# Kernel optimization log

Hardware: AMD Instinct MI355X
Metric: run time of the kernel (lower is better)

## Reference

```python
import jax, jax.numpy as jnp
import numpy as np

SEQ, BATCH, IN, H = 188, 256, 128, 256


def _lstm_scan(x_proj, w_hh, batch, hidden):
    # x_proj: (T, B, 4H) = input projection + biases, already computed
    h0 = jnp.zeros((batch, hidden), x_proj.dtype)
    c0 = jnp.zeros((batch, hidden), x_proj.dtype)
    w_hh_t = w_hh.T  # (H, 4H)

    def step(carry, xt):
        h, c = carry
        gates = xt + h @ w_hh_t  # (B, 4H)
        i, f, g, o = jnp.split(gates, 4, axis=-1)  # PyTorch gate order i,f,g,o
        i = jax.nn.sigmoid(i)
        f = jax.nn.sigmoid(f)
        g = jnp.tanh(g)
        o = jax.nn.sigmoid(o)
        c = f * c + i * g
        h = o * jnp.tanh(c)
        return (h, c), h

    _, hs = jax.lax.scan(step, (h0, c0), x_proj)
    return hs  # (T, B, H)


def setup_inputs() -> dict:
    key = jax.random.key(0)
    ks = jax.random.split(key, 9)
    s = 1.0 / np.sqrt(H)  # PyTorch default init scale
    mk = lambda k, shape: jax.random.uniform(k, shape, jnp.float32, -s, s)
    return {
        "x": jax.random.normal(ks[0], (SEQ, BATCH, IN), jnp.float32),
        "w_ih_f": mk(ks[1], (4 * H, IN)),
        "w_hh_f": mk(ks[2], (4 * H, H)),
        "b_ih_f": mk(ks[3], (4 * H,)),
        "b_hh_f": mk(ks[4], (4 * H,)),
        "w_ih_b": mk(ks[5], (4 * H, IN)),
        "w_hh_b": mk(ks[6], (4 * H, H)),
        "b_ih_b": mk(ks[7], (4 * H,)),
        "b_hh_b": mk(ks[8], (4 * H,)),
    }


def reference(x, w_ih_f, w_hh_f, b_ih_f, b_hh_f, w_ih_b, w_hh_b, b_ih_b, b_hh_b):
    batch = x.shape[1]
    # Precompute input projections for all timesteps (big GEMM outside the scan)
    xp_f = jnp.einsum('tbi,gi->tbg', x, w_ih_f) + b_ih_f + b_hh_f
    xp_b = jnp.einsum('tbi,gi->tbg', x[::-1], w_ih_b) + b_ih_b + b_hh_b
    out_f = _lstm_scan(xp_f, w_hh_f, batch, H)            # (T, B, H)
    out_b = _lstm_scan(xp_b, w_hh_b, batch, H)[::-1]      # reversed back
    return jnp.concatenate([out_f, out_b], axis=-1)       # (T, B, 2H)
```

## Files before the change

kernel.cpp:

```cpp
#include <hip/hip_runtime.h>

#define T_SEQ 188
#define NB    256
#define NIN   128
#define NH    256
#define SCQ   (0.0625f / 16129.0f)

typedef __attribute__((ext_vector_type(8))) short s16x8;
typedef __attribute__((ext_vector_type(4))) short s16x4;
typedef __attribute__((ext_vector_type(4))) float f32x4;
typedef __attribute__((ext_vector_type(4))) int   i32x4;

__device__ __forceinline__ short f2bf(float f) {
    union { float f; unsigned u; } v; v.f = f;
    unsigned r = v.u + 0x7fffu + ((v.u >> 16) & 1u);
    return (short)(r >> 16);
}
__device__ __forceinline__ float bf2f(unsigned short s) {
    union { unsigned u; float f; } t; t.u = ((unsigned)s) << 16; return t.f;
}
__device__ __forceinline__ float sigf(float x) {
    return __builtin_amdgcn_rcpf(1.0f + __expf(-x));
}
__device__ __forceinline__ float tanh_(float x) {
    return 1.0f - 2.0f * __builtin_amdgcn_rcpf(__expf(2.0f * x) + 1.0f);
}

__device__ __forceinline__ void lds_barrier() {
    asm volatile("s_waitcnt lgkmcnt(0)" ::: "memory");
    __builtin_amdgcn_s_barrier();
    asm volatile("" ::: "memory");
}

__global__ __launch_bounds__(256) void xp_gemm(
    const float* __restrict__ x,
    const float* __restrict__ w_ih_f, const float* __restrict__ w_ih_b,
    const float* __restrict__ b_ih_f, const float* __restrict__ b_hh_f,
    const float* __restrict__ b_ih_b, const float* __restrict__ b_hh_b,
    unsigned short* __restrict__ xp)
{
    const int mt = blockIdx.x >> 1;
    const int d  = blockIdx.x & 1;
    const int t  = mt >> 2, b0 = (mt & 3) * 64;
    const float* w_ih = d ? w_ih_b : w_ih_f;
    const float* b_ih = d ? b_ih_b : b_ih_f;
    const float* b_hh = d ? b_hh_b : b_hh_f;
    const int tid = threadIdx.x;
    const int v = tid >> 6, l = tid & 63, lg = l >> 4, lb = l & 15;

    __shared__ short wl[64][136];
    __shared__ float biasS[1024];

    #pragma unroll
    for (int j = 0; j < 4; ++j) {
        const int g = tid * 4 + j * 1024; (void)g;
    }
    {
        const int g = tid * 4;
        float4 bi = *(const float4*)(b_ih + g);
        float4 bh = *(const float4*)(b_hh + g);
        biasS[g + 0] = bi.x + bh.x; biasS[g + 1] = bi.y + bh.y;
        biasS[g + 2] = bi.z + bh.z; biasS[g + 3] = bi.w + bh.w;
    }

    s16x8 a[4];
    {
        const float* xr = x + ((size_t)(t * NB + b0 + 16 * v + lb)) * NIN + 8 * lg;
        #pragma unroll
        for (int kk = 0; kk < 4; ++kk) {
            float4 p0 = *(const float4*)(xr + 32 * kk);
            float4 p1 = *(const float4*)(xr + 32 * kk + 4);
            s16x8 tv;
            tv[0] = f2bf(p0.x); tv[1] = f2bf(p0.y); tv[2] = f2bf(p0.z); tv[3] = f2bf(p0.w);
            tv[4] = f2bf(p1.x); tv[5] = f2bf(p1.y); tv[6] = f2bf(p1.z); tv[7] = f2bf(p1.w);
            a[kk] = tv;
        }
    }

    const int wr = tid >> 2, wk = (tid & 3) * 32;

    unsigned short* xpb =
        xp + ((size_t)(d * T_SEQ + t) * NB + b0 + 16 * v + 4 * lg) * 1024 + lb;

    for (int nt = 0; nt < 16; ++nt) {
        const int Nb = nt * 64;
        {
            const float* wsrc = w_ih + ((size_t)(Nb + wr)) * NIN + wk;
            #pragma unroll
            for (int j = 0; j < 4; ++j) {
                float4 p0 = *(const float4*)(wsrc + 8 * j);
                float4 p1 = *(const float4*)(wsrc + 8 * j + 4);
                s16x8 tv;
                tv[0] = f2bf(p0.x); tv[1] = f2bf(p0.y); tv[2] = f2bf(p0.z); tv[3] = f2bf(p0.w);
                tv[4] = f2bf(p1.x); tv[5] = f2bf(p1.y); tv[6] = f2bf(p1.z); tv[7] = f2bf(p1.w);
                *(s16x8*)&wl[wr][wk + 8 * j] = tv;
            }
        }
        __syncthreads();

        f32x4 acc[4];
        #pragma unroll
        for (int nf = 0; nf < 4; ++nf) {
            const float bs = biasS[Nb + nf * 16 + lb];
            acc[nf][0] = bs; acc[nf][1] = bs; acc[nf][2] = bs; acc[nf][3] = bs;
        }
        #pragma unroll
        for (int kk = 0; kk < 4; ++kk)
            #pragma unroll
            for (int nf = 0; nf < 4; ++nf) {
                s16x8 bf_ = *(const s16x8*)&wl[nf * 16 + lb][kk * 32 + 8 * lg];
                acc[nf] = __builtin_amdgcn_mfma_f32_16x16x32_bf16(a[kk], bf_, acc[nf], 0, 0, 0);
            }
        __syncthreads();

        #pragma unroll
        for (int nf = 0; nf < 4; ++nf)
            #pragma unroll
            for (int rr = 0; rr < 4; ++rr)
                xpb[(size_t)rr * 1024 + Nb + nf * 16] = (unsigned short)f2bf(acc[nf][rr]);
    }
}

__device__ __forceinline__ void lstm_step(
    int p, int w, int l, int lg, int lb, int c, int huq, int hwb,
    const unsigned short*& xpp, long dxp, float*& outp, long dout,
    int* hl, int (&rscr)[16][4][4][16],
    const i32x4 (&wq)[4][4], float& cst,
    unsigned short (&cur)[4], unsigned short (&nxt)[4])
{
    #pragma unroll
    for (int G = 0; G < 4; ++G)
        nxt[G] = xpp[G * 256];
    xpp += dxp;

    i32x4 ac[4];
    #pragma unroll
    for (int G = 0; G < 4; ++G) {
        ac[G][0] = 0; ac[G][1] = 0; ac[G][2] = 0; ac[G][3] = 0;
    }
    #pragma unroll
    for (int kk = 0; kk < 4; ++kk) {
        i32x4 bq = *(const i32x4*)&hl[p * 1024 + kk * 256 + 4 * l];
        ac[0] = __builtin_amdgcn_mfma_i32_16x16x64_i8(wq[0][kk], bq, ac[0], 0, 0, 0);
        ac[1] = __builtin_amdgcn_mfma_i32_16x16x64_i8(wq[1][kk], bq, ac[1], 0, 0, 0);
        ac[2] = __builtin_amdgcn_mfma_i32_16x16x64_i8(wq[2][kk], bq, ac[2], 0, 0, 0);
        ac[3] = __builtin_amdgcn_mfma_i32_16x16x64_i8(wq[3][kk], bq, ac[3], 0, 0, 0);
    }

    if (lb < 4) {
        #pragma unroll
        for (int G = 0; G < 4; ++G)
            *(i32x4*)&rscr[w][G][lb][4 * lg] = ac[G];
    }
    asm volatile("s_waitcnt lgkmcnt(0)" ::: "memory");
    int av[4];
    #pragma unroll
    for (int G = 0; G < 4; ++G)
        av[G] = rscr[w][G][c][huq];
    asm volatile("s_waitcnt lgkmcnt(0)" ::: "memory");

    const float gi = SCQ * (float)av[0] + bf2f(cur[0]);
    const float gf = SCQ * (float)av[1] + bf2f(cur[1]);
    const float gg = SCQ * (float)av[2] + bf2f(cur[2]);
    const float go = SCQ * (float)av[3] + bf2f(cur[3]);
    const float iv = sigf(gi), fv = sigf(gf);
    const float gv = tanh_(gg), ov = sigf(go);
    const float cc = fv * cst + iv * gv;
    cst = cc;
    const float h = ov * tanh_(cc);
    *outp = h;
    outp += dout;
    ((signed char*)hl)[(p ^ 1) * 4096 + hwb] = (signed char)(int)rintf(h * 127.0f);

    lds_barrier();
}

__global__ __launch_bounds__(1024, 4) void lstm_rec(
    const float* __restrict__ w_hh_f, const float* __restrict__ w_hh_b,
    const unsigned short* __restrict__ xp, float* __restrict__ out)
{
    const int bid = blockIdx.x;
    const int d  = bid >> 6;
    const int bt = bid & 63;
    const float* w_hh = d ? w_hh_b : w_hh_f;
    const int tid = threadIdx.x;
    const int w = tid >> 6, l = tid & 63, lg = l >> 4, lb = l & 15;
    const int c = l & 3, huq = l >> 2;

    __shared__ int hl[2 * 1024];
    __shared__ int rscr[16][4][4][16];

    i32x4 wq[4][4];
    #pragma unroll
    for (int G = 0; G < 4; ++G) {
        const int row = G * 256 + 16 * w + lb;
        #pragma unroll
        for (int kk = 0; kk < 4; ++kk) {
            i32x4 pk;
            #pragma unroll
            for (int r = 0; r < 4; ++r) {
                float4 wv = *(const float4*)(w_hh + (size_t)row * NH + kk * 64 + 16 * lg + 4 * r);
                const int q0 = (int)rintf(wv.x * 2032.0f) & 255;
                const int q1 = (int)rintf(wv.y * 2032.0f) & 255;
                const int q2 = (int)rintf(wv.z * 2032.0f) & 255;
                const int q3 = (int)rintf(wv.w * 2032.0f) & 255;
                pk[r] = q0 | (q1 << 8) | (q2 << 16) | (q3 << 24);
            }
            wq[G][kk] = pk;
        }
    }
    for (int i = tid; i < 2048; i += 1024) hl[i] = 0;

    const int hu = 16 * w + huq;
    const int hwb = (hu >> 6) * 1024 + ((hu >> 4) & 3) * 256 + c * 16 + (hu & 15);

    float cst = 0.f;
    unsigned short XPA[4], XPB[4];
    const int t0 = d ? (T_SEQ - 1) : 0;
    const long dxp  = (d ? -(long)NB : (long)NB) * 1024;
    const long dout = (d ? -(long)NB : (long)NB) * 512;
    const unsigned short* xpp =
        xp + ((size_t)(d * T_SEQ + t0) * NB + bt * 4 + c) * 1024 + hu;
    float* outp = out + ((size_t)t0 * NB + bt * 4 + c) * 512 + d * 256 + hu;
    #pragma unroll
    for (int G = 0; G < 4; ++G)
        XPA[G] = xpp[G * 256];
    xpp += dxp;
    __syncthreads();

    for (int s2 = 0; s2 < T_SEQ / 2; ++s2) {
        lstm_step(0, w, l, lg, lb, c, huq, hwb, xpp, dxp, outp, dout,
                  hl, rscr, wq, cst, XPA, XPB);
        lstm_step(1, w, l, lg, lb, c, huq, hwb, xpp, dxp, outp, dout,
                  hl, rscr, wq, cst, XPB, XPA);
    }
}

#define ZSTR_FB 392
__global__ __launch_bounds__(512, 2) void lstm_fb(
    const float* __restrict__ x,
    const float* __restrict__ w_ih_f, const float* __restrict__ w_hh_f,
    const float* __restrict__ b_ih_f, const float* __restrict__ b_hh_f,
    const float* __restrict__ w_ih_b, const float* __restrict__ w_hh_b,
    const float* __restrict__ b_ih_b, const float* __restrict__ b_hh_b,
    float* __restrict__ out, unsigned* __restrict__ flags)
{
    const int b  = blockIdx.x;
    const int d  = b >> 5;
    const int hh = (b >> 4) & 1;
    const int bt = b & 15;
    const int pb = b ^ 16;
    const int po = 1 - hh;
    const float* w_ih = d ? w_ih_b : w_ih_f;
    const float* w_hh = d ? w_hh_b : w_hh_f;
    const float* b_ih = d ? b_ih_b : b_ih_f;
    const float* b_hh = d ? b_hh_b : b_hh_f;
    const int tid = threadIdx.x;
    const int w = tid >> 6, l = tid & 63, lg = l >> 4, lb = l & 15;
    const int hbase = hh * 128 + 16 * w;

    __shared__ short Z[2][16][ZSTR_FB];
    __shared__ float biasL[8][4][16];
    const int off_x   = lg * 8;
    const int off_own = (4 + 4 * hh) * 32 + lg * 8;
    const int off_par = (4 + 4 * po) * 32 + lg * 8;

    s16x8 wf[4][12];
    #pragma unroll
    for (int G = 0; G < 4; ++G) {
        const int gc = G * 256 + hbase + lb;
        #pragma unroll
        for (int kkidx = 0; kkidx < 12; ++kkidx) {
            const int kb = (kkidx < 4) ? (off_x + 32 * kkidx)
                         : (kkidx < 8) ? (off_own + 32 * (kkidx - 4))
                                       : (off_par + 32 * (kkidx - 8));
            const float* src = (kb < NIN) ? (w_ih + (size_t)gc * NIN + kb)
                                          : (w_hh + (size_t)gc * NH + (kb - NIN));
            float4 a  = *(const float4*)(src);
            float4 b2 = *(const float4*)(src + 4);
            s16x8 tv;
            tv[0] = f2bf(a.x);  tv[1] = f2bf(a.y);  tv[2] = f2bf(a.z);  tv[3] = f2bf(a.w);
            tv[4] = f2bf(b2.x); tv[5] = f2bf(b2.y); tv[6] = f2bf(b2.z); tv[7] = f2bf(b2.w);
            wf[G][kkidx] = tv;
        }
    }
    {
        const int G = lb >> 2, r = lb & 3;
        const int gcr = G * 256 + hbase + 4 * lg + r;
        biasL[w][G][4 * lg + r] = b_ih[gcr] + b_hh[gcr];
    }
    const int srow = tid >> 5;
    const int sk4  = (tid & 31) * 4;
    {
        s16x8 zz;
        #pragma unroll
        for (int i = 0; i < 8; ++i) zz[i] = 0;
        *(s16x8*)&Z[0][srow][NIN + (tid & 31) * 8] = zz;
        const int t0 = d ? (T_SEQ - 1) : 0;
        float4 xv0 = *(const float4*)(x + ((size_t)(t0 * NB + bt * 16 + srow)) * NIN + sk4);
        s16x4 xp_;
        xp_[0] = f2bf(xv0.x); xp_[1] = f2bf(xv0.y); xp_[2] = f2bf(xv0.z); xp_[3] = f2bf(xv0.w);
        *(s16x4*)&Z[0][srow][sk4] = xp_;
    }
    float cst[4] = {0.f, 0.f, 0.f, 0.f};
    __syncthreads();
    unsigned* myflag = flags + b * 16;
    unsigned* pflag  = flags + pb * 16;
    float* outp = out + (size_t)(bt * 16) * 512 + d * 256 + hbase + 4 * lg;

    for (int s = 0; s < T_SEQ; ++s) {
        const int p = s & 1;
        const int t = d ? (T_SEQ - 1 - s) : s;
        float4 xv;
        const bool havex = (s + 1 < T_SEQ);
        if (havex) {
            const int tn = d ? (T_SEQ - 2 - s) : (s + 1);
            xv = *(const float4*)(x + ((size_t)(tn * NB + bt * 16 + srow)) * NIN + sk4);
        }
        f32x4 acc[4];
        #pragma unroll
        for (int G = 0; G < 4; ++G)
            acc[G] = *(const f32x4*)&biasL[w][G][4 * lg];
        const short* zrow = &Z[p][lb][0];
        #pragma unroll
        for (int kk = 0; kk < 4; ++kk) {
            s16x8 bfv = *(const s16x8*)(zrow + off_x + 32 * kk);
            acc[0] = __builtin_amdgcn_mfma_f32_16x16x32_bf16(wf[0][kk], bfv, acc[0], 0, 0, 0);
            acc[1] = __builtin_amdgcn_mfma_f32_16x16x32_bf16(wf[1][kk], bfv, acc[1], 0, 0, 0);
            acc[2] = __builtin_amdgcn_mfma_f32_16x16x32_bf16(wf[2][kk], bfv, acc[2], 0, 0, 0);
            acc[3] = __builtin_amdgcn_mfma_f32_16x16x32_bf16(wf[3][kk], bfv, acc[3], 0, 0, 0);
        }
        #pragma unroll
        for (int kk = 0; kk < 4; ++kk) {
            s16x8 bfv = *(const s16x8*)(zrow + off_own + 32 * kk);
            acc[0] = __builtin_amdgcn_mfma_f32_16x16x32_bf16(wf[0][4 + kk], bfv, acc[0], 0, 0, 0);
            acc[1] = __builtin_amdgcn_mfma_f32_16x16x32_bf16(wf[1][4 + kk], bfv, acc[1], 0, 0, 0);
            acc[2] = __builtin_amdgcn_mfma_f32_16x16x32_bf16(wf[2][4 + kk], bfv, acc[2], 0, 0, 0);
            acc[3] = __builtin_amdgcn_mfma_f32_16x16x32_bf16(wf[3][4 + kk], bfv, acc[3], 0, 0, 0);
        }
        if (s > 0) {
            const unsigned want = (unsigned)s;
            while (__hip_atomic_load(pflag, __ATOMIC_RELAXED, __HIP_MEMORY_SCOPE_AGENT) < want)
                __builtin_amdgcn_s_sleep(1);
            __builtin_amdgcn_fence(__ATOMIC_ACQUIRE, "agent");
            const int tprev = d ? (T_SEQ - s) : (s - 1);
            float4 pv = *(const float4*)(out + (size_t)tprev * NB * 512
                         + (size_t)(bt * 16 + srow) * 512 + d * 256 + po * 128 + sk4);
            s16x4 pp;
            pp[0] = f2bf(pv.x); pp[1] = f2bf(pv.y); pp[2] = f2bf(pv.z); pp[3] = f2bf(pv.w);
            *(s16x4*)&Z[p][srow][NIN + po * 128 + sk4] = pp;
        }
        __syncthreads();
        #pragma unroll
        for (int kk = 0; kk < 4; ++kk) {
            s16x8 bfv = *(const s16x8*)(zrow + off_par + 32 * kk);
            acc[0] = __builtin_amdgcn_mfma_f32_16x16x32_bf16(wf[0][8 + kk], bfv, acc[0], 0, 0, 0);
            acc[1] = __builtin_amdgcn_mfma_f32_16x16x32_bf16(wf[1][8 + kk], bfv, acc[1], 0, 0, 0);
            acc[2] = __builtin_amdgcn_mfma_f32_16x16x32_bf16(wf[2][8 + kk], bfv, acc[2], 0, 0, 0);
            acc[3] = __builtin_amdgcn_mfma_f32_16x16x32_bf16(wf[3][8 + kk], bfv, acc[3], 0, 0, 0);
        }
        float4 hout; s16x4 hbf;
        #pragma unroll
        for (int r = 0; r < 4; ++r) {
            const float iv = sigf(acc[0][r]);
            const float fv = sigf(acc[1][r]);
            const float gv = tanh_(acc[2][r]);
            const float ov = sigf(acc[3][r]);
            const float cc = fv * cst[r] + iv * gv;
            cst[r] = cc;
            const float h = ov * tanh_(cc);
            (&hout.x)[r] = h;
            hbf[r] = f2bf(h);
        }
        *(s16x4*)&Z[p ^ 1][lb][NIN + hbase + 4 * lg] = hbf;
        if (havex) {
            s16x4 xp_;
            xp_[0] = f2bf(xv.x); xp_[1] = f2bf(xv.y); xp_[2] = f2bf(xv.z); xp_[3] = f2bf(xv.w);
            *(s16x4*)&Z[p ^ 1][srow][sk4] = xp_;
        }
        *(f32x4*)(outp + (size_t)t * NB * 512 + lb * 512) = *(f32x4*)&hout;
        __syncthreads();
        if (tid == 0 && s + 1 < T_SEQ)
            __hip_atomic_store(myflag, (unsigned)(s + 1),
                               __ATOMIC_RELEASE, __HIP_MEMORY_SCOPE_AGENT);
    }
}

extern "C" void kernel_launch(void* const* d_in, const int* in_sizes, int n_in,
                              void* d_out, int out_size, void* d_ws, size_t ws_size,
                              hipStream_t stream) {
    const float* x      = (const float*)d_in[0];
    const float* w_ih_f = (const float*)d_in[1];
    const float* w_hh_f = (const float*)d_in[2];
    const float* b_ih_f = (const float*)d_in[3];
    const float* b_hh_f = (const float*)d_in[4];
    const float* w_ih_b = (const float*)d_in[5];
    const float* w_hh_b = (const float*)d_in[6];
    const float* b_ih_b = (const float*)d_in[7];
    const float* b_hh_b = (const float*)d_in[8];
    float* out = (float*)d_out;

    const size_t XPN = (size_t)2 * T_SEQ * NB * 1024;

    if (ws_size >= XPN * 2) {
        unsigned short* xp = (unsigned short*)d_ws;
        xp_gemm<<<dim3(752 * 2), dim3(256), 0, stream>>>(
            x, w_ih_f, w_ih_b, b_ih_f, b_hh_f, b_ih_b, b_hh_b, xp);
        lstm_rec<<<dim3(128), dim3(1024), 0, stream>>>(w_hh_f, w_hh_b, xp, out);
    } else {
        unsigned* flags = (unsigned*)d_ws;
        hipMemsetAsync(flags, 0, 4096, stream);
        lstm_fb<<<dim3(64), dim3(512), 0, stream>>>(
            x, w_ih_f, w_hh_f, b_ih_f, b_hh_f, w_ih_b, w_hh_b, b_ih_b, b_hh_b,
            out, flags);
    }
}
```

Measured before the change: 346.3 us.

## Fuse input-projection GEMM into recurrent kernel with flag-based producer/consumer overlap

Merges the separate xp_gemm and lstm_rec launches into one kernel. The first 128 blocks run the recurrence, and the remaining blocks compute input projections in time order for each direction. Producers publish per-timestep, per-batch-group flags, and recurrent blocks spin-wait on them in chunks of 32 steps, so the GEMM overlaps the serial recurrence instead of running before it. It also stages the GEMM output through LDS so global stores are coalesced. The cost is a memset plus polling overhead, and the scheme relies on the 128 recurrent blocks being co-resident with the producers to avoid deadlock. GEMM blocks now launch 1024 threads while only 256 do work, so they waste occupancy.

Measured after the change: 522.3 us. 1.51x slower.

```diff
diff --git a/kernel.cpp b/kernel.cpp
--- a/kernel.cpp
+++ b/kernel.cpp
@@ -5,6 +5,7 @@
 #define NIN   128
 #define NH    256
 #define SCQ   (0.0625f / 16129.0f)
+#define NREC  128
 
 typedef __attribute__((ext_vector_type(8))) short s16x8;
 typedef __attribute__((ext_vector_type(4))) short s16x4;
@@ -25,106 +26,16 @@
 __device__ __forceinline__ float tanh_(float x) {
     return 1.0f - 2.0f * __builtin_amdgcn_rcpf(__expf(2.0f * x) + 1.0f);
 }
-
 __device__ __forceinline__ void lds_barrier() {
     asm volatile("s_waitcnt lgkmcnt(0)" ::: "memory");
     __builtin_amdgcn_s_barrier();
     asm volatile("" ::: "memory");
 }
 
-__global__ __launch_bounds__(256) void xp_gemm(
-    const float* __restrict__ x,
-    const float* __restrict__ w_ih_f, const float* __restrict__ w_ih_b,
-    const float* __restrict__ b_ih_f, const float* __restrict__ b_hh_f,
-    const float* __restrict__ b_ih_b, const float* __restrict__ b_hh_b,
-    unsigned short* __restrict__ xp)
-{
-    const int mt = blockIdx.x >> 1;
-    const int d  = blockIdx.x & 1;
-    const int t  = mt >> 2, b0 = (mt & 3) * 64;
-    const float* w_ih = d ? w_ih_b : w_ih_f;
-    const float* b_ih = d ? b_ih_b : b_ih_f;
-    const float* b_hh = d ? b_hh_b : b_hh_f;
-    const int tid = threadIdx.x;
-    const int v = tid >> 6, l = tid & 63, lg = l >> 4, lb = l & 15;
-
-    __shared__ short wl[64][136];
-    __shared__ float biasS[1024];
-
-    #pragma unroll
-    for (int j = 0; j < 4; ++j) {
-        const int g = tid * 4 + j * 1024; (void)g;
-    }
-    {
-        const int g = tid * 4;
-        float4 bi = *(const float4*)(b_ih + g);
-        float4 bh = *(const float4*)(b_hh + g);
-        biasS[g + 0] = bi.x + bh.x; biasS[g + 1] = bi.y + bh.y;
-        biasS[g + 2] = bi.z + bh.z; biasS[g + 3] = bi.w + bh.w;
-    }
-
-    s16x8 a[4];
-    {
-        const float* xr = x + ((size_t)(t * NB + b0 + 16 * v + lb)) * NIN + 8 * lg;
-        #pragma unroll
-        for (int kk = 0; kk < 4; ++kk) {
-            float4 p0 = *(const float4*)(xr + 32 * kk);
-            float4 p1 = *(const float4*)(xr + 32 * kk + 4);
-            s16x8 tv;
-            tv[0] = f2bf(p0.x); tv[1] = f2bf(p0.y); tv[2] = f2bf(p0.z); tv[3] = f2bf(p0.w);
-            tv[4] = f2bf(p1.x); tv[5] = f2bf(p1.y); tv[6] = f2bf(p1.z); tv[7] = f2bf(p1.w);
-            a[kk] = tv;
-        }
-    }
-
-    const int wr = tid >> 2, wk = (tid & 3) * 32;
-
-    unsigned short* xpb =
-        xp + ((size_t)(d * T_SEQ + t) * NB + b0 + 16 * v + 4 * lg) * 1024 + lb;
-
-    for (int nt = 0; nt < 16; ++nt) {
-        const int Nb = nt * 64;
-        {
-            const float* wsrc = w_ih + ((size_t)(Nb + wr)) * NIN + wk;
-            #pragma unroll
-            for (int j = 0; j < 4; ++j) {
-                float4 p0 = *(const float4*)(wsrc + 8 * j);
-                float4 p1 = *(const float4*)(wsrc + 8 * j + 4);
-                s16x8 tv;
-                tv[0] = f2bf(p0.x); tv[1] = f2bf(p0.y); tv[2] = f2bf(p0.z); tv[3] = f2bf(p0.w);
-                tv[4] = f2bf(p1.x); tv[5] = f2bf(p1.y); tv[6] = f2bf(p1.z); tv[7] = f2bf(p1.w);
-                *(s16x8*)&wl[wr][wk + 8 * j] = tv;
-            }
-        }
-        __syncthreads();
-
-        f32x4 acc[4];
-        #pragma unroll
-        for (int nf = 0; nf < 4; ++nf) {
-            const float bs = biasS[Nb + nf * 16 + lb];
-            acc[nf][0] = bs; acc[nf][1] = bs; acc[nf][2] = bs; acc[nf][3] = bs;
-        }
-        #pragma unroll
-        for (int kk = 0; kk < 4; ++kk)
-            #pragma unroll
-            for (int nf = 0; nf < 4; ++nf) {
-                s16x8 bf_ = *(const s16x8*)&wl[nf * 16 + lb][kk * 32 + 8 * lg];
-                acc[nf] = __builtin_amdgcn_mfma_f32_16x16x32_bf16(a[kk], bf_, acc[nf], 0, 0, 0);
-            }
-        __syncthreads();
-
-        #pragma unroll
-        for (int nf = 0; nf < 4; ++nf)
-            #pragma unroll
-            for (int rr = 0; rr < 4; ++rr)
-                xpb[(size_t)rr * 1024 + Nb + nf * 16] = (unsigned short)f2bf(acc[nf][rr]);
-    }
-}
-
 __device__ __forceinline__ void lstm_step(
     int p, int w, int l, int lg, int lb, int c, int huq, int hwb,
     const unsigned short*& xpp, long dxp, float*& outp, long dout,
-    int* hl, int (&rscr)[16][4][4][16],
+    int* hl, int (*rscr)[4][4][16],
     const i32x4 (&wq)[4][4], float& cst,
     unsigned short (&cur)[4], unsigned short (&nxt)[4])
 {
@@ -175,20 +86,127 @@
     lds_barrier();
 }
 
-__global__ __launch_bounds__(1024, 4) void lstm_rec(
-    const float* __restrict__ w_hh_f, const float* __restrict__ w_hh_b,
-    const unsigned short* __restrict__ xp, float* __restrict__ out)
+__global__ __launch_bounds__(1024, 4) void lstm_fused(
+    const float* __restrict__ x,
+    const float* __restrict__ w_ih_f, const float* __restrict__ w_hh_f,
+    const float* __restrict__ b_ih_f, const float* __restrict__ b_hh_f,
+    const float* __restrict__ w_ih_b, const float* __restrict__ w_hh_b,
+    const float* __restrict__ b_ih_b, const float* __restrict__ b_hh_b,
+    unsigned short* __restrict__ xp, int* __restrict__ flags,
+    float* __restrict__ out)
 {
+    __shared__ char smem[30208];
     const int bid = blockIdx.x;
+    const int tid = threadIdx.x;
+
+    if (bid >= NREC) {
+        const int gid = bid - NREC;
+        const int d   = gid & 1;
+        const int mt  = gid >> 1;
+        const int tseq = mt >> 2, g = mt & 3;
+        const int t   = d ? (T_SEQ - 1 - tseq) : tseq;
+        const int b0  = g * 64;
+        const float* w_ih = d ? w_ih_b : w_ih_f;
+        const float* b_ih = d ? b_ih_b : b_ih_f;
+        const float* b_hh = d ? b_hh_b : b_hh_f;
+
+        if (tid >= 256) {
+            for (int i = 0; i < 33; ++i) __syncthreads();
+            return;
+        }
+
+        short (*wl)[136]  = (short(*)[136])smem;
+        short (*xo)[68]   = (short(*)[68])(smem + 17408);
+        float* biasS      = (float*)(smem + 26112);
+
+        const int v = tid >> 6, l = tid & 63, lg = l >> 4, lb = l & 15;
+        {
+            const int gg4 = tid * 4;
+            float4 bi = *(const float4*)(b_ih + gg4);
+            float4 bh = *(const float4*)(b_hh + gg4);
+            biasS[gg4 + 0] = bi.x + bh.x; biasS[gg4 + 1] = bi.y + bh.y;
+            biasS[gg4 + 2] = bi.z + bh.z; biasS[gg4 + 3] = bi.w + bh.w;
+        }
+        s16x8 a[4];
+        {
+            const float* xr = x + ((size_t)(t * NB + b0 + 16 * v + lb)) * NIN + 8 * lg;
+            #pragma unroll
+            for (int kk = 0; kk < 4; ++kk) {
+                float4 p0 = *(const float4*)(xr + 32 * kk);
+                float4 p1 = *(const float4*)(xr + 32 * kk + 4);
+                s16x8 tv;
+                tv[0] = f2bf(p0.x); tv[1] = f2bf(p0.y); tv[2] = f2bf(p0.z); tv[3] = f2bf(p0.w);
+                tv[4] = f2bf(p1.x); tv[5] = f2bf(p1.y); tv[6] = f2bf(p1.z); tv[7] = f2bf(p1.w);
+                a[kk] = tv;
+            }
+        }
+        const int wr = tid >> 2, wk = (tid & 3) * 32;
+        const int orow = tid >> 2, oko = (tid & 3) * 16;
+
+        for (int nt = 0; nt < 16; ++nt) {
+            const int Nb = nt * 64;
+            {
+                const float* wsrc = w_ih + ((size_t)(Nb + wr)) * NIN + wk;
+                #pragma unroll
+                for (int j = 0; j < 4; ++j) {
+                    float4 p0 = *(const float4*)(wsrc + 8 * j);
+                    float4 p1 = *(const float4*)(wsrc + 8 * j + 4);
+                    s16x8 tv;
+                    tv[0] = f2bf(p0.x); tv[1] = f2bf(p0.y); tv[2] = f2bf(p0.z); tv[3] = f2bf(p0.w);
+                    tv[4] = f2bf(p1.x); tv[5] = f2bf(p1.y); tv[6] = f2bf(p1.z); tv[7] = f2bf(p1.w);
+                    *(s16x8*)&wl[wr][wk + 8 * j] = tv;
+                }
+            }
+            __syncthreads();
+            f32x4 acc[4];
+            #pragma unroll
+            for (int nf = 0; nf < 4; ++nf) {
+                const float bs = biasS[Nb + nf * 16 + lb];
+                acc[nf][0] = bs; acc[nf][1] = bs; acc[nf][2] = bs; acc[nf][3] = bs;
+            }
+            #pragma unroll
+            for (int kk = 0; kk < 4; ++kk)
+                #pragma unroll
+                for (int nf = 0; nf < 4; ++nf) {
+                    s16x8 bf_ = *(const s16x8*)&wl[nf * 16 + lb][kk * 32 + 8 * lg];
+                    acc[nf] = __builtin_amdgcn_mfma_f32_16x16x32_bf16(a[kk], bf_, acc[nf], 0, 0, 0);
+                }
+            #pragma unroll
+            for (int nf = 0; nf < 4; ++nf)
+                #pragma unroll
+                for (int rr = 0; rr < 4; ++rr)
+                    xo[16 * v + 4 * lg + rr][nf * 16 + lb] = f2bf(acc[nf][rr]);
+            __syncthreads();
+            {
+                s16x8 v0 = *(const s16x8*)&xo[orow][oko];
+                s16x8 v1 = *(const s16x8*)&xo[orow][oko + 8];
+                unsigned short* dst = xp + ((size_t)(d * T_SEQ + t) * NB + b0 + orow) * 1024
+                                         + Nb + oko;
+                union { s16x8 s; i32x4 i; } u0, u1; u0.s = v0; u1.s = v1;
+                asm volatile("global_store_dwordx4 %0, %1, off sc0 sc1"
+                             :: "v"(dst), "v"(u0.i) : "memory");
+                asm volatile("global_store_dwordx4 %0, %1, off sc0 sc1"
+                             :: "v"(dst + 8), "v"(u1.i) : "memory");
+            }
+        }
+        __syncthreads();
+        if (tid == 0) {
+            int* fp = flags + (d * T_SEQ + t) * 4 + g;
+            unsigned one = 1;
+            asm volatile("global_store_dword %0, %1, off sc0 sc1"
+                         :: "v"(fp), "v"(one) : "memory");
+        }
+        return;
+    }
+
     const int d  = bid >> 6;
     const int bt = bid & 63;
     const float* w_hh = d ? w_hh_b : w_hh_f;
-    const int tid = threadIdx.x;
     const int w = tid >> 6, l = tid & 63, lg = l >> 4, lb = l & 15;
     const int c = l & 3, huq = l >> 2;
 
-    __shared__ int hl[2 * 1024];
-    __shared__ int rscr[16][4][4][16];
+    int* hl = (int*)smem;
+    int (*rscr)[4][4][16] = (int(*)[4][4][16])(smem + 8192);
 
     i32x4 wq[4][4];
     #pragma unroll
@@ -222,6 +240,30 @@
     const unsigned short* xpp =
         xp + ((size_t)(d * T_SEQ + t0) * NB + bt * 4 + c) * 1024 + hu;
     float* outp = out + ((size_t)t0 * NB + bt * 4 + c) * 512 + d * 256 + hu;
+
+    const int fgrp = bt >> 4;
+    #define CHUNK_WAIT(S)                                                          \
+    do {                                                                           \
+        if (tid == 0) {                                                            \
+            int ulim = (S) + 32; if (ulim > T_SEQ - 1) ulim = T_SEQ - 1;           \
+            for (int u = (S); u <= ulim; ++u) {                                    \
+                const int tt = d ? (T_SEQ - 1 - u) : u;                            \
+                const int* fp = flags + (d * T_SEQ + tt) * 4 + fgrp;               \
+                unsigned fv;                                                       \
+                while (true) {                                                     \
+                    asm volatile("global_load_dword %0, %1, off sc0 sc1\n\t"       \
+                                 "s_waitcnt vmcnt(0)"                              \
+                                 : "=v"(fv) : "v"(fp) : "memory");                 \
+                    if (fv) break;                                                 \
+                    __builtin_amdgcn_s_sleep(16);                                  \
+                }                                                                  \
+            }                                                                      \
+            __builtin_amdgcn_fence(__ATOMIC_ACQUIRE, "agent");                     \
+        }                                                                          \
+        lds_barrier();                                                             \
+    } while (0)
+
+    CHUNK_WAIT(0);
     #pragma unroll
     for (int G = 0; G < 4; ++G)
         XPA[G] = xpp[G * 256];
@@ -229,11 +271,14 @@
     __syncthreads();
 
     for (int s2 = 0; s2 < T_SEQ / 2; ++s2) {
+        if ((s2 & 15) == 0 && s2)
+            CHUNK_WAIT(2 * s2);
         lstm_step(0, w, l, lg, lb, c, huq, hwb, xpp, dxp, outp, dout,
                   hl, rscr, wq, cst, XPA, XPB);
         lstm_step(1, w, l, lg, lb, c, huq, hwb, xpp, dxp, outp, dout,
                   hl, rscr, wq, cst, XPB, XPA);
     }
+    #undef CHUNK_WAIT
 }
 
 #define ZSTR_FB 392
@@ -400,13 +445,15 @@
     const float* b_hh_b = (const float*)d_in[8];
     float* out = (float*)d_out;
 
-    const size_t XPN = (size_t)2 * T_SEQ * NB * 1024;
-
-    if (ws_size >= XPN * 2) {
+    const size_t XPB = (size_t)2 * T_SEQ * NB * 1024 * 2;
+
+    if (ws_size >= XPB + 8192) {
         unsigned short* xp = (unsigned short*)d_ws;
-        xp_gemm<<<dim3(752 * 2), dim3(256), 0, stream>>>(
-            x, w_ih_f, w_ih_b, b_ih_f, b_hh_f, b_ih_b, b_hh_b, xp);
-        lstm_rec<<<dim3(128), dim3(1024), 0, stream>>>(w_hh_f, w_hh_b, xp, out);
+        int* flags = (int*)((char*)d_ws + XPB);
+        hipMemsetAsync(flags, 0, 2 * T_SEQ * 4 * sizeof(int), stream);
+        lstm_fused<<<dim3(NREC + 1504), dim3(1024), 0, stream>>>(
+            x, w_ih_f, w_hh_f, b_ih_f, b_hh_f, w_ih_b, w_hh_b, b_ih_b, b_hh_b,
+            xp, flags, out);
     } else {
         unsigned* flags = (unsigned*)d_ws;
         hipMemsetAsync(flags, 0, 4096, stream);
```

## Pre-swizzle bf16 input weights, double-buffer LDS tiles, coalesce xp stores via LDS

Applied to the files above, without the earlier changes.

Adds a small prepass kernel that converts w_ih to bf16 once, in the exact MFMA fragment order, so each xp_gemm block copies ready-made tiles instead of reconverting fp32 weights for every one of its 16 N-tiles. Weight tiles are double-buffered in LDS, with the next tile prefetched into registers while the current one is multiplied. Output is staged through an LDS tile so each thread writes 16-byte vectors instead of scattered 2-byte stores. The costs are an extra kernel launch, more LDS per block, and a required workspace increase that can fall back to the slower path if the workspace is too small.

Measured after the change: 286.8 us. 1.21x faster.

```diff
diff --git a/kernel.cpp b/kernel.cpp
--- a/kernel.cpp
+++ b/kernel.cpp
@@ -25,16 +25,37 @@
 __device__ __forceinline__ float tanh_(float x) {
     return 1.0f - 2.0f * __builtin_amdgcn_rcpf(__expf(2.0f * x) + 1.0f);
 }
-
 __device__ __forceinline__ void lds_barrier() {
     asm volatile("s_waitcnt lgkmcnt(0)" ::: "memory");
     __builtin_amdgcn_s_barrier();
     asm volatile("" ::: "memory");
 }
 
+__global__ __launch_bounds__(256) void wconv(
+    const float* __restrict__ w_ih_f, const float* __restrict__ w_ih_b,
+    unsigned short* __restrict__ wswz)
+{
+    const int j = blockIdx.x * 256 + threadIdx.x;
+    const int d  = j >> 14;
+    const int r  = j & 16383;
+    const int nt = r >> 10;
+    const int rr = r & 1023;
+    const int q  = rr >> 6;
+    const int l  = rr & 63;
+    const int nf = q >> 2, kk = q & 3;
+    const int gate = nt * 64 + nf * 16 + (l & 15);
+    const int kb   = kk * 32 + 8 * (l >> 4);
+    const float* src = (d ? w_ih_b : w_ih_f) + (size_t)gate * NIN + kb;
+    float4 p0 = *(const float4*)(src);
+    float4 p1 = *(const float4*)(src + 4);
+    s16x8 tv;
+    tv[0] = f2bf(p0.x); tv[1] = f2bf(p0.y); tv[2] = f2bf(p0.z); tv[3] = f2bf(p0.w);
+    tv[4] = f2bf(p1.x); tv[5] = f2bf(p1.y); tv[6] = f2bf(p1.z); tv[7] = f2bf(p1.w);
+    *(s16x8*)(wswz + (size_t)j * 8) = tv;
+}
+
 __global__ __launch_bounds__(256) void xp_gemm(
-    const float* __restrict__ x,
-    const float* __restrict__ w_ih_f, const float* __restrict__ w_ih_b,
+    const float* __restrict__ x, const unsigned short* __restrict__ wswz,
     const float* __restrict__ b_ih_f, const float* __restrict__ b_hh_f,
     const float* __restrict__ b_ih_b, const float* __restrict__ b_hh_b,
     unsigned short* __restrict__ xp)
@@ -42,25 +63,21 @@
     const int mt = blockIdx.x >> 1;
     const int d  = blockIdx.x & 1;
     const int t  = mt >> 2, b0 = (mt & 3) * 64;
-    const float* w_ih = d ? w_ih_b : w_ih_f;
     const float* b_ih = d ? b_ih_b : b_ih_f;
     const float* b_hh = d ? b_hh_b : b_hh_f;
     const int tid = threadIdx.x;
     const int v = tid >> 6, l = tid & 63, lg = l >> 4, lb = l & 15;
 
-    __shared__ short wl[64][136];
+    __shared__ short wl[2][8192];
+    __shared__ short xo[64][68];
     __shared__ float biasS[1024];
 
-    #pragma unroll
-    for (int j = 0; j < 4; ++j) {
-        const int g = tid * 4 + j * 1024; (void)g;
-    }
     {
-        const int g = tid * 4;
-        float4 bi = *(const float4*)(b_ih + g);
-        float4 bh = *(const float4*)(b_hh + g);
-        biasS[g + 0] = bi.x + bh.x; biasS[g + 1] = bi.y + bh.y;
-        biasS[g + 2] = bi.z + bh.z; biasS[g + 3] = bi.w + bh.w;
+        const int g4 = tid * 4;
+        float4 bi = *(const float4*)(b_ih + g4);
+        float4 bh = *(const float4*)(b_hh + g4);
+        biasS[g4 + 0] = bi.x + bh.x; biasS[g4 + 1] = bi.y + bh.y;
+        biasS[g4 + 2] = bi.z + bh.z; biasS[g4 + 3] = bi.w + bh.w;
     }
 
     s16x8 a[4];
@@ -77,47 +94,58 @@
         }
     }
 
-    const int wr = tid >> 2, wk = (tid & 3) * 32;
-
-    unsigned short* xpb =
-        xp + ((size_t)(d * T_SEQ + t) * NB + b0 + 16 * v + 4 * lg) * 1024 + lb;
+    const unsigned short* wbase = wswz + (size_t)d * 131072;
+    s16x8 stg[4];
+    #pragma unroll
+    for (int i = 0; i < 4; ++i)
+        stg[i] = *(const s16x8*)(wbase + ((size_t)(tid + 256 * i)) * 8);
+    #pragma unroll
+    for (int i = 0; i < 4; ++i)
+        *(s16x8*)&wl[0][(tid + 256 * i) * 8] = stg[i];
+    __syncthreads();
+
+    unsigned short* xrow =
+        xp + ((size_t)(d * T_SEQ + t) * NB + b0 + (tid >> 2)) * 1024 + (tid & 3) * 16;
 
     for (int nt = 0; nt < 16; ++nt) {
-        const int Nb = nt * 64;
-        {
-            const float* wsrc = w_ih + ((size_t)(Nb + wr)) * NIN + wk;
+        const int cur = nt & 1;
+        if (nt + 1 < 16) {
             #pragma unroll
-            for (int j = 0; j < 4; ++j) {
-                float4 p0 = *(const float4*)(wsrc + 8 * j);
-                float4 p1 = *(const float4*)(wsrc + 8 * j + 4);
-                s16x8 tv;
-                tv[0] = f2bf(p0.x); tv[1] = f2bf(p0.y); tv[2] = f2bf(p0.z); tv[3] = f2bf(p0.w);
-                tv[4] = f2bf(p1.x); tv[5] = f2bf(p1.y); tv[6] = f2bf(p1.z); tv[7] = f2bf(p1.w);
-                *(s16x8*)&wl[wr][wk + 8 * j] = tv;
-            }
-        }
-        __syncthreads();
-
+            for (int i = 0; i < 4; ++i)
+                stg[i] = *(const s16x8*)(wbase + ((size_t)(nt + 1) * 8192)
+                                               + ((size_t)(tid + 256 * i)) * 8);
+        }
         f32x4 acc[4];
         #pragma unroll
         for (int nf = 0; nf < 4; ++nf) {
-            const float bs = biasS[Nb + nf * 16 + lb];
+            const float bs = biasS[nt * 64 + nf * 16 + lb];
             acc[nf][0] = bs; acc[nf][1] = bs; acc[nf][2] = bs; acc[nf][3] = bs;
         }
         #pragma unroll
         for (int kk = 0; kk < 4; ++kk)
             #pragma unroll
             for (int nf = 0; nf < 4; ++nf) {
-                s16x8 bf_ = *(const s16x8*)&wl[nf * 16 + lb][kk * 32 + 8 * lg];
+                s16x8 bf_ = *(const s16x8*)&wl[cur][((nf * 4 + kk) * 64 + l) * 8];
                 acc[nf] = __builtin_amdgcn_mfma_f32_16x16x32_bf16(a[kk], bf_, acc[nf], 0, 0, 0);
             }
-        __syncthreads();
-
         #pragma unroll
         for (int nf = 0; nf < 4; ++nf)
             #pragma unroll
             for (int rr = 0; rr < 4; ++rr)
-                xpb[(size_t)rr * 1024 + Nb + nf * 16] = (unsigned short)f2bf(acc[nf][rr]);
+                xo[16 * v + 4 * lg + rr][nf * 16 + lb] = f2bf(acc[nf][rr]);
+        lds_barrier();
+        {
+            s16x8 o0 = *(const s16x8*)&xo[tid >> 2][(tid & 3) * 16];
+            s16x8 o1 = *(const s16x8*)&xo[tid >> 2][(tid & 3) * 16 + 8];
+            *(s16x8*)(xrow + nt * 64)     = o0;
+            *(s16x8*)(xrow + nt * 64 + 8) = o1;
+        }
+        if (nt + 1 < 16) {
+            #pragma unroll
+            for (int i = 0; i < 4; ++i)
+                *(s16x8*)&wl[cur ^ 1][(tid + 256 * i) * 8] = stg[i];
+        }
+        lds_barrier();
     }
 }
 
@@ -400,12 +428,15 @@
     const float* b_hh_b = (const float*)d_in[8];
     float* out = (float*)d_out;
 
-    const size_t XPN = (size_t)2 * T_SEQ * NB * 1024;
-
-    if (ws_size >= XPN * 2) {
-        unsigned short* xp = (unsigned short*)d_ws;
+    const size_t XPB = (size_t)2 * T_SEQ * NB * 1024 * 2;
+    const size_t WSW = (size_t)32768 * 16;
+
+    if (ws_size >= XPB + WSW) {
+        unsigned short* xp   = (unsigned short*)d_ws;
+        unsigned short* wswz = (unsigned short*)((char*)d_ws + XPB);
+        wconv<<<dim3(128), dim3(256), 0, stream>>>(w_ih_f, w_ih_b, wswz);
         xp_gemm<<<dim3(752 * 2), dim3(256), 0, stream>>>(
-            x, w_ih_f, w_ih_b, b_ih_f, b_hh_f, b_ih_b, b_hh_b, xp);
+            x, wswz, b_ih_f, b_hh_f, b_ih_b, b_hh_b, xp);
         lstm_rec<<<dim3(128), dim3(1024), 0, stream>>>(w_hh_f, w_hh_b, xp, out);
     } else {
         unsigned* flags = (unsigned*)d_ws;
```
